# Optimization experiments

Measured on AMD Instinct MI355X. Metric: run time of the kernel, lower is better.

The kernel has to match this reference:

```python
import jax, jax.numpy as jnp
import numpy as np

NL = 5      # number of Block_mamba layers
DM = 256    # d_model
DI = 512    # d_inner = expand * d_model
DS = 64     # d_state
DTR = 16    # dt_rank = ceil(d_model / 16)
HID = 1024  # FFN hidden = dim * mlp_ratio


def layernorm(x, w, b):
    mu = jnp.mean(x, axis=-1, keepdims=True)
    var = jnp.mean((x - mu) ** 2, axis=-1, keepdims=True)
    return (x - mu) * jax.lax.rsqrt(var + 1e-5) * w + b


def mamba_fwd(x, inw, cw, cb, xpw, dtw, dtb, alog, Dp, ow):
    # x: [B, L, DM]
    B, L, _ = x.shape
    xz = jnp.einsum('blc,dc->bld', x, inw)            # [B, L, 2*DI]
    xi, z = xz[..., :DI], xz[..., DI:]
    # causal depthwise conv1d, kernel size 2 (d_conv=2)
    xprev = jnp.pad(xi, ((0, 0), (1, 0), (0, 0)))[:, :-1]
    xc = jax.nn.silu(xi * cw[:, 1] + xprev * cw[:, 0] + cb)   # [B, L, DI]
    xdbl = jnp.einsum('bld,ed->ble', xc, xpw)         # [B, L, DTR+2*DS]
    dt = jax.nn.softplus(jnp.einsum('blr,dr->bld', xdbl[..., :DTR], dtw) + dtb)  # [B,L,DI]
    Bm = xdbl[..., DTR:DTR + DS]                      # [B, L, DS]
    Cm = xdbl[..., DTR + DS:]                         # [B, L, DS]
    A = -jnp.exp(alog)                                # [DI, DS]

    def step(h, inp):
        dt_t, B_t, C_t, u_t = inp                     # [B,DI],[B,DS],[B,DS],[B,DI]
        h = jnp.exp(dt_t[:, :, None] * A) * h + dt_t[:, :, None] * B_t[:, None, :] * u_t[:, :, None]
        y = jnp.einsum('bds,bs->bd', h, C_t)
        return h, y

    h0 = jnp.zeros((B, DI, DS), x.dtype)
    xs = (dt.transpose(1, 0, 2), Bm.transpose(1, 0, 2), Cm.transpose(1, 0, 2), xc.transpose(1, 0, 2))
    _, ys = jax.lax.scan(step, h0, xs)                # ys: [L, B, DI]
    y = ys.transpose(1, 0, 2) + xc * Dp
    y = y * jax.nn.silu(z)
    return jnp.einsum('bld,cd->blc', y, ow)           # [B, L, DM]


def setup_inputs() -> dict:
    key = jax.random.key(0)
    ks = jax.random.split(key, 16)
    f32 = jnp.float32
    d = {}
    d['x'] = jax.random.normal(ks[0], (8, 4096, DM), dtype=f32)
    d['in_proj_w'] = jax.random.normal(ks[1], (NL, 2 * DI, DM), dtype=f32) * 0.02
    d['conv_w'] = jax.random.normal(ks[2], (NL, DI, 2), dtype=f32) * 0.2
    d['conv_b'] = jnp.zeros((NL, DI), f32)
    d['x_proj_w'] = jax.random.normal(ks[3], (NL, DTR + 2 * DS, DI), dtype=f32) * 0.02
    d['dt_proj_w'] = jax.random.normal(ks[4], (NL, DI, DTR), dtype=f32) * 0.02
    d['dt_proj_b'] = jax.random.normal(ks[5], (NL, DI), dtype=f32) * 0.1 - 4.0
    d['A_log'] = jnp.broadcast_to(jnp.log(jnp.arange(1, DS + 1, dtype=f32)), (NL, DI, DS)).copy()
    d['D'] = jnp.ones((NL, DI), f32)
    d['out_proj_w'] = jax.random.normal(ks[6], (NL, DM, DI), dtype=f32) * 0.02
    d['norm1_w'] = jnp.ones((NL, DM), f32)
    d['norm1_b'] = jnp.zeros((NL, DM), f32)
    d['norm2_w'] = jnp.ones((NL, DM), f32)
    d['norm2_b'] = jnp.zeros((NL, DM), f32)
    d['fc1_w'] = jax.random.normal(ks[7], (NL, HID, DM), dtype=f32) * 0.02
    d['fc1_b'] = jnp.zeros((NL, HID), f32)
    d['fc2_w'] = jax.random.normal(ks[8], (NL, DM, HID), dtype=f32) * 0.02
    d['fc2_b'] = jnp.zeros((NL, DM), f32)
    return d


def reference(x, in_proj_w, conv_w, conv_b, x_proj_w, dt_proj_w, dt_proj_b, A_log, D,
              out_proj_w, norm1_w, norm1_b, norm2_w, norm2_b, fc1_w, fc1_b, fc2_w, fc2_b):
    for i in range(NL):
        xn = layernorm(x, norm1_w[i], norm1_b[i])
        args = (in_proj_w[i], conv_w[i], conv_b[i], x_proj_w[i], dt_proj_w[i],
                dt_proj_b[i], A_log[i], D[i], out_proj_w[i])
        fwd = mamba_fwd(xn, *args)
        bwd = mamba_fwd(xn[:, ::-1], *args)[:, ::-1]
        x = x + fwd + bwd                      # bidirectional residual (shared weights)
        xn2 = layernorm(x, norm2_w[i], norm2_b[i])
        h = jax.nn.gelu(jnp.einsum('blc,hc->blh', xn2, fc1_w[i]) + fc1_b[i], approximate=False)
        x = x + jnp.einsum('blh,ch->blc', h, fc2_w[i]) + fc2_b[i]
    return x
```

## Files before the change

### kernel.cpp

```cpp
#include <hip/hip_runtime.h>
#include <hip/hip_bf16.h>
#include <math.h>
#include <stdint.h>

#define NLAY 5
#define DM 256
#define DI 512
#define DS 64
#define DTR 16
#define HID 1024
#define BB 8
#define LSEQ 4096
#define RR (BB*LSEQ)
#define NCH 32
#define CL (LSEQ/NCH)
#define LOG2E 1.4426950408889634f

typedef __hip_bfloat16 bf16;
typedef float vf2 __attribute__((ext_vector_type(2)));
typedef float vf4 __attribute__((ext_vector_type(4)));
typedef unsigned int vu4 __attribute__((ext_vector_type(4)));

__device__ __forceinline__ float silu_f(float x) {
    return x / (1.0f + __expf(-x));
}
__device__ __forceinline__ float gelu_f(float x) {
    return 0.5f * x * (1.0f + erff(x * 0.70710678118654752f));
}
__device__ __forceinline__ float softplus_f(float x) {
    return fmaxf(x, 0.0f) + log1pf(__expf(-fabsf(x)));
}
__device__ __forceinline__ float to_f(bf16 x) { return __bfloat162float(x); }
__device__ __forceinline__ unsigned short bf_bits(float v) {
    bf16 h = __float2bfloat16(v);
    return *reinterpret_cast<unsigned short*>(&h);
}
__device__ __forceinline__ float bflo(uint32_t w) { return __uint_as_float(w << 16); }
__device__ __forceinline__ float rawhi(uint32_t w) { return __uint_as_float(w); }

#define HIDX(dir,b,c,s,d) (((((size_t)(dir)*BB+(b))*NCH+(c))*DS+(s))*DI+(d))
#define SIDX(dir,b,c,d)   ((((size_t)(dir)*BB+(b))*NCH+(c))*DI+(d))

__global__ void ln_kernel(const float* __restrict__ x, const float* __restrict__ w,
                          const float* __restrict__ b, bf16* __restrict__ out) {
    int wave = threadIdx.x >> 6;
    int lane = threadIdx.x & 63;
    int row  = blockIdx.x * 4 + wave;
    const float4* xr = (const float4*)(x + (size_t)row * DM);
    float4 v = xr[lane];
    float s  = v.x + v.y + v.z + v.w;
    float sq = v.x*v.x + v.y*v.y + v.z*v.z + v.w*v.w;
    #pragma unroll
    for (int off = 32; off; off >>= 1) {
        s  += __shfl_xor(s,  off);
        sq += __shfl_xor(sq, off);
    }
    float mu  = s * (1.0f / DM);
    float var = sq * (1.0f / DM) - mu * mu;
    float rs  = rsqrtf(var + 1e-5f);
    float4 wv = ((const float4*)w)[lane];
    float4 bv = ((const float4*)b)[lane];
    ushort4 o;
    o.x = bf_bits((v.x - mu) * rs * wv.x + bv.x);
    o.y = bf_bits((v.y - mu) * rs * wv.y + bv.y);
    o.z = bf_bits((v.z - mu) * rs * wv.z + bv.z);
    o.w = bf_bits((v.w - mu) * rs * wv.w + bv.w);
    ((ushort4*)(out + (size_t)row * DM))[lane] = o;
}

__global__ void wconv_kernel(const float* __restrict__ a0, const float* __restrict__ a1,
                             const float* __restrict__ a2, const float* __restrict__ a3,
                             const float* __restrict__ a4, bf16* __restrict__ out) {
    size_t i = (size_t)blockIdx.x * 256 + threadIdx.x;
    const float* src; size_t off;
    if (i < 262144)      { src = a0; off = i; }
    else if (i < 335872) { src = a1; off = i - 262144; }
    else if (i < 466944) { src = a2; off = i - 335872; }
    else if (i < 729088) { src = a3; off = i - 466944; }
    else                 { src = a4; off = i - 729088; }
    out[i] = __float2bfloat16(src[off]);
}

template<int ACT, bool ACCUM, bool BIAS, typename TC>
__global__ __launch_bounds__(256)
void mfma_gemm(const bf16* __restrict__ A, const bf16* __restrict__ W,
               const float* __restrict__ bias, TC* __restrict__ C,
               int M, int N, int K) {
    __shared__ bf16 As[128][40];
    __shared__ bf16 Ws[64][40];
    int tid = threadIdx.x;
    int m0 = blockIdx.x * 128;
    int n0 = blockIdx.y * 64;
    int w  = tid >> 6, lane = tid & 63;
    int wr = w >> 1, wc = w & 1;
    int fr = lane & 15;
    int kg = lane >> 4;
    vf4 acc[4][2] = {};

    int sr = tid >> 2;
    int skc = (tid & 3) * 8;
    for (int k0 = 0; k0 < K; k0 += 32) {
        #pragma unroll
        for (int i = 0; i < 2; i++) {
            int q = tid + i * 256;
            int r = q >> 2, kc = (q & 3) * 8;
            *(vu4*)&As[r][kc] = *(const vu4*)&A[(size_t)(m0 + r) * K + k0 + kc];
        }
        {
            int n = n0 + sr;
            vu4 v = {0u, 0u, 0u, 0u};
            if (n < N) v = *(const vu4*)&W[(size_t)n * K + k0 + skc];
            *(vu4*)&Ws[sr][skc] = v;
        }
        __syncthreads();
        vu4 af[4], bw[2];
        #pragma unroll
        for (int m = 0; m < 4; m++)
            af[m] = *(const vu4*)&As[wr * 64 + m * 16 + fr][kg * 8];
        #pragma unroll
        for (int n = 0; n < 2; n++)
            bw[n] = *(const vu4*)&Ws[wc * 32 + n * 16 + fr][kg * 8];
        #pragma unroll
        for (int m = 0; m < 4; m++)
            #pragma unroll
            for (int n = 0; n < 2; n++)
                asm("v_mfma_f32_16x16x32_bf16 %0, %1, %2, %0"
                    : "+v"(acc[m][n]) : "v"(af[m]), "v"(bw[n]));
        __syncthreads();
    }

    #pragma unroll
    for (int m = 0; m < 4; m++) {
        #pragma unroll
        for (int n = 0; n < 2; n++) {
            int col = n0 + wc * 32 + n * 16 + fr;
            if (col >= N) continue;
            float bz = BIAS ? bias[col] : 0.0f;
            #pragma unroll
            for (int r = 0; r < 4; r++) {
                int row = m0 + wr * 64 + m * 16 + kg * 4 + r;
                float v = acc[m][n][r] + bz;
                if (ACT == 1) v = silu_f(v);
                else if (ACT == 2) v = gelu_f(v);
                if constexpr (sizeof(TC) == 2) {
                    ((bf16*)C)[(size_t)row * N + col] = __float2bfloat16(v);
                } else {
                    float* cp = (float*)C + (size_t)row * N + col;
                    if (ACCUM) *cp += v; else *cp = v;
                }
            }
        }
    }
}

__global__ void conv_kernel(const bf16* __restrict__ xi, const float* __restrict__ cw,
                            const float* __restrict__ cb, bf16* __restrict__ xcf,
                            bf16* __restrict__ xcb) {
    size_t idx = (size_t)blockIdx.x * 256 + threadIdx.x;
    int d = (int)(idx & (DI - 1));
    size_t row = idx >> 9;
    int t = (int)(row & (LSEQ - 1));
    float x0   = to_f(xi[idx]);
    float prev = (t > 0)        ? to_f(xi[idx - DI]) : 0.0f;
    float nxt  = (t < LSEQ - 1) ? to_f(xi[idx + DI]) : 0.0f;
    float w0 = cw[d * 2], w1 = cw[d * 2 + 1], bc = cb[d];
    float base = x0 * w1 + bc;
    xcf[idx] = __float2bfloat16(silu_f(base + prev * w0));
    xcb[idx] = __float2bfloat16(silu_f(base + nxt * w0));
}

__global__ void dt_kernel(const bf16* __restrict__ xdbl, const float* __restrict__ dtw,
                          const float* __restrict__ dtb, bf16* __restrict__ dt) {
    __shared__ float sx[DTR];
    size_t row = blockIdx.x;
    int d = threadIdx.x;
    if (d < DTR) sx[d] = to_f(xdbl[row * 144 + d]);
    __syncthreads();
    float acc = dtb[d];
    #pragma unroll
    for (int r = 0; r < DTR; r++) acc += sx[r] * dtw[d * DTR + r];
    dt[row * DI + d] = __float2bfloat16(softplus_f(acc));
}


__global__ __launch_bounds__(256) void scanA_kernel(
        const bf16* __restrict__ dt2, const bf16* __restrict__ xdbl2,
        const bf16* __restrict__ xcf, const bf16* __restrict__ xcb,
        bf16* __restrict__ hbuf, float* __restrict__ sdtbuf) {
    int wv = blockIdx.x * 4 + (threadIdx.x >> 6);
    int lane = threadIdx.x & 63;
    int dh  = wv & 15;
    int c   = (wv >> 4) & 31;
    int b   = (wv >> 9) & 7;
    int dir = wv >> 12;
    int dl  = lane & 31;
    int sh  = lane >> 5;
    int d   = dh * 32 + dl;
    const bf16* dt = dt2 + (size_t)dir * RR * DI;
    const bf16* xc = dir ? xcb : xcf;
    const bf16* xb = xdbl2 + (size_t)dir * RR * 144;

    size_t row0 = (size_t)b * LSEQ + (dir ? ((c + 1) * CL - 1) : (c * CL));
    const bf16* dtp = dt + row0 * DI + d;
    const bf16* up  = xc + row0 * DI + d;
    const uint32_t* bcp = (const uint32_t*)(xb + row0 * 144 + DTR) + sh * 16;
    intptr_t stepDI = dir ? -DI : DI;
    intptr_t stepBC = dir ? -72 : 72;

    vf2 h[16];
    #pragma unroll
    for (int j = 0; j < 16; j++) h[j] = (vf2)0.0f;
    float sdt = 0.0f;

    for (int it = 0; it < CL; ++it) {
        float dtv = to_f(*dtp);
        float u   = to_f(*up);
        float du  = dtv * u;
        sdt += dtv;
        float rho = __builtin_amdgcn_exp2f(-dtv * LOG2E);
        float r2 = rho * rho, r3 = r2 * rho, r4 = r2 * r2;
        float r5 = r4 * rho, r6 = r4 * r2, r7 = r4 * r3, r8 = r4 * r4;
        float r16 = r8 * r8, r32 = r16 * r16;
        float sf = sh ? r32 : 1.0f;
        vf2 sf2 = {sf, sf};
        vf2 e0 = vf2{rho, r2} * sf2;
        vf2 e1 = vf2{r3, r4} * sf2;
        vf2 e2 = vf2{r5, r6} * sf2;
        vf2 e3 = vf2{r7, r8} * sf2;
        vf2 r8p = {r8, r8};
        vf2 du2 = {du, du};
        const vu4* pB = (const vu4*)bcp;
        #pragma unroll
        for (int i = 0; i < 4; i++) {
            vu4 w = pB[i];
            vf2 b0 = {bflo(w.x), rawhi(w.x)};
            vf2 b1 = {bflo(w.y), rawhi(w.y)};
            vf2 b2 = {bflo(w.z), rawhi(w.z)};
            vf2 b3 = {bflo(w.w), rawhi(w.w)};
            h[4*i]   = e0 * h[4*i]   + du2 * b0;
            h[4*i+1] = e1 * h[4*i+1] + du2 * b1;
            h[4*i+2] = e2 * h[4*i+2] + du2 * b2;
            h[4*i+3] = e3 * h[4*i+3] + du2 * b3;
            e0 *= r8p; e1 *= r8p; e2 *= r8p; e3 *= r8p;
        }
        dtp += stepDI; up += stepDI; bcp += stepBC;
    }
    size_t base = HIDX(dir, b, c, 0, d) + (size_t)(sh * 32) * DI;
    #pragma unroll
    for (int j = 0; j < 16; j++) {
        hbuf[base + (size_t)(2*j)   * DI] = __float2bfloat16(h[j].x);
        hbuf[base + (size_t)(2*j+1) * DI] = __float2bfloat16(h[j].y);
    }
    if (sh == 0) sdtbuf[SIDX(dir, b, c, d)] = sdt;
}

__global__ __launch_bounds__(64) void scanB_kernel(
        bf16* __restrict__ hbuf, const float* __restrict__ sdtbuf) {
    int x = blockIdx.x;
    int dsl = x & 7;
    int s   = (x >> 3) & 63;
    int b   = (x >> 9) & 7;
    int dir = x >> 12;
    int d = dsl * 64 + threadIdx.x;
    float kexp = -(float)(s + 1) * LOG2E;
    float h0 = 0.0f;
    for (int i = 0; i < NCH; ++i) {
        int c = dir ? (NCH - 1 - i) : i;
        size_t hi = HIDX(dir, b, c, s, d);
        float E  = __builtin_amdgcn_exp2f(kexp * sdtbuf[SIDX(dir, b, c, d)]);
        float hf = to_f(hbuf[hi]);
        hbuf[hi] = __float2bfloat16(h0);
        h0 = E * h0 + hf;
    }
}

__global__ __launch_bounds__(256) void scanC_kernel(
        const bf16* __restrict__ dt2, const bf16* __restrict__ xdbl2,
        bf16* __restrict__ xcf, bf16* __restrict__ xcb,
        const float* __restrict__ Dp, const bf16* __restrict__ hbuf) {
    int wv = blockIdx.x * 4 + (threadIdx.x >> 6);
    int lane = threadIdx.x & 63;
    int dh  = wv & 15;
    int c   = (wv >> 4) & 31;
    int b   = (wv >> 9) & 7;
    int dir = wv >> 12;
    int dl  = lane & 31;
    int sh  = lane >> 5;
    int d   = dh * 32 + dl;
    const bf16* dt = dt2 + (size_t)dir * RR * DI;
    bf16* xc = dir ? xcb : xcf;
    const bf16* xb = xdbl2 + (size_t)dir * RR * 144;
    float Dv = Dp[d];

    size_t row0 = (size_t)b * LSEQ + (dir ? ((c + 1) * CL - 1) : (c * CL));
    const bf16* dtp = dt + row0 * DI + d;
    bf16* up = xc + row0 * DI + d;
    const uint32_t* bcp = (const uint32_t*)(xb + row0 * 144 + DTR) + sh * 16;
    intptr_t stepDI = dir ? -DI : DI;
    intptr_t stepBC = dir ? -72 : 72;

    vf2 h[16];
    size_t base = HIDX(dir, b, c, 0, d) + (size_t)(sh * 32) * DI;
    #pragma unroll
    for (int j = 0; j < 16; j++) {
        h[j].x = to_f(hbuf[base + (size_t)(2*j)   * DI]);
        h[j].y = to_f(hbuf[base + (size_t)(2*j+1) * DI]);
    }

    for (int it = 0; it < CL; ++it) {
        float dtv = to_f(*dtp);
        float u   = to_f(*up);
        float du  = dtv * u;
        float rho = __builtin_amdgcn_exp2f(-dtv * LOG2E);
        float r2 = rho * rho, r3 = r2 * rho, r4 = r2 * r2;
        float r5 = r4 * rho, r6 = r4 * r2, r7 = r4 * r3, r8 = r4 * r4;
        float r16 = r8 * r8, r32 = r16 * r16;
        float sf = sh ? r32 : 1.0f;
        vf2 sf2 = {sf, sf};
        vf2 e0 = vf2{rho, r2} * sf2;
        vf2 e1 = vf2{r3, r4} * sf2;
        vf2 e2 = vf2{r5, r6} * sf2;
        vf2 e3 = vf2{r7, r8} * sf2;
        vf2 r8p = {r8, r8};
        vf2 du2 = {du, du};
        vf2 y0 = (vf2)0.0f, y1 = (vf2)0.0f;
        const vu4* pB = (const vu4*)bcp;
        const vu4* pC = (const vu4*)(bcp + 32);
        #pragma unroll
        for (int i = 0; i < 4; i++) {
            vu4 wB = pB[i];
            vu4 wC = pC[i];
            vf2 b0 = {bflo(wB.x), rawhi(wB.x)};
            vf2 b1 = {bflo(wB.y), rawhi(wB.y)};
            vf2 b2 = {bflo(wB.z), rawhi(wB.z)};
            vf2 b3 = {bflo(wB.w), rawhi(wB.w)};
            vf2 c0 = {bflo(wC.x), rawhi(wC.x)};
            vf2 c1 = {bflo(wC.y), rawhi(wC.y)};
            vf2 c2 = {bflo(wC.z), rawhi(wC.z)};
            vf2 c3 = {bflo(wC.w), rawhi(wC.w)};
            h[4*i]   = e0 * h[4*i]   + du2 * b0;  y0 += h[4*i]   * c0;
            h[4*i+1] = e1 * h[4*i+1] + du2 * b1;  y1 += h[4*i+1] * c1;
            h[4*i+2] = e2 * h[4*i+2] + du2 * b2;  y0 += h[4*i+2] * c2;
            h[4*i+3] = e3 * h[4*i+3] + du2 * b3;  y1 += h[4*i+3] * c3;
            e0 *= r8p; e1 *= r8p; e2 *= r8p; e3 *= r8p;
        }
        vf2 yp = y0 + y1;
        float yhalf = yp.x + yp.y;
        float y = yhalf + __shfl_xor(yhalf, 32);
        if (sh == 0) *up = __float2bfloat16(y + u * Dv);
        dtp += stepDI; up += stepDI; bcp += stepBC;
    }
}

__global__ void combine_kernel(bf16* __restrict__ xcf, const bf16* __restrict__ xcb,
                               const bf16* __restrict__ z) {
    size_t idx = (size_t)blockIdx.x * 256 + threadIdx.x;
    int dcol = (int)(idx & (DI - 1));
    size_t row = idx >> 9;
    float zz = to_f(z[row * DI + dcol]);
    float v = (to_f(xcf[idx]) + to_f(xcb[idx])) * silu_f(zz);
    xcf[idx] = __float2bfloat16(v);
}

extern "C" void kernel_launch(void* const* d_in, const int* in_sizes, int n_in,
                              void* d_out, int out_size, void* d_ws, size_t ws_size,
                              hipStream_t stream) {
    const float* x_in = (const float*)d_in[0];
    const float* inw  = (const float*)d_in[1];
    const float* cw   = (const float*)d_in[2];
    const float* cb   = (const float*)d_in[3];
    const float* xpw  = (const float*)d_in[4];
    const float* dtw  = (const float*)d_in[5];
    const float* dtb  = (const float*)d_in[6];
    const float* Dp   = (const float*)d_in[8];
    const float* ow   = (const float*)d_in[9];
    const float* n1w  = (const float*)d_in[10];
    const float* n1b  = (const float*)d_in[11];
    const float* n2w  = (const float*)d_in[12];
    const float* n2b  = (const float*)d_in[13];
    const float* f1w  = (const float*)d_in[14];
    const float* f1b  = (const float*)d_in[15];
    const float* f2w  = (const float*)d_in[16];
    const float* f2b  = (const float*)d_in[17];

    const size_t SZ_DI  = (size_t)RR * DI * 2;
    const size_t SZ_XDB = (size_t)2 * RR * 144 * 2;
    const size_t SZ_DT  = (size_t)2 * RR * DI * 2;
    const size_t SZ_WBF = (size_t)991232 * 2;
    const size_t SZ_SDT = (size_t)2 * BB * NCH * DI * 4;
    const size_t NEEDED = 4 * SZ_DI + SZ_XDB + SZ_DT + SZ_WBF + SZ_SDT;
    if (ws_size < NEEDED) return;

    char* p = (char*)d_ws;
    bf16*  xi    = (bf16*)p; p += SZ_DI;
    bf16*  z     = (bf16*)p; p += SZ_DI;
    bf16*  xcf   = (bf16*)p; p += SZ_DI;
    bf16*  xcb   = (bf16*)p; p += SZ_DI;
    bf16*  xdbl2 = (bf16*)p; p += SZ_XDB;
    bf16*  dt2   = (bf16*)p; p += SZ_DT;
    bf16*  wbf   = (bf16*)p; p += SZ_WBF;
    float* sdtb  = (float*)p; p += SZ_SDT;
    bf16*  hbuf  = xi;
    bf16*  xn    = xcb;
    bf16*  hmlp  = dt2;
    bf16*  inw_bf = wbf;
    bf16*  xpw_bf = wbf + 262144;
    bf16*  ow_bf  = wbf + 335872;
    bf16*  f1w_bf = wbf + 466944;
    bf16*  f2w_bf = wbf + 729088;

    float* x = (float*)d_out;
    hipMemcpyAsync(x, x_in, (size_t)RR * DM * sizeof(float), hipMemcpyDeviceToDevice, stream);

    dim3 blk(256);
    for (int l = 0; l < NLAY; ++l) {
        const float* inw_l = inw + (size_t)l * 2 * DI * DM;
        const float* cw_l  = cw  + (size_t)l * DI * 2;
        const float* cb_l  = cb  + (size_t)l * DI;
        const float* xpw_l = xpw + (size_t)l * 144 * DI;
        const float* dtw_l = dtw + (size_t)l * DI * DTR;
        const float* dtb_l = dtb + (size_t)l * DI;
        const float* Dp_l  = Dp  + (size_t)l * DI;
        const float* ow_l  = ow  + (size_t)l * DM * DI;
        const float* f1w_l = f1w + (size_t)l * HID * DM;
        const float* f1b_l = f1b + (size_t)l * HID;
        const float* f2w_l = f2w + (size_t)l * DM * HID;
        const float* f2b_l = f2b + (size_t)l * DM;

        wconv_kernel<<<3872, blk, 0, stream>>>(inw_l, xpw_l, ow_l, f1w_l, f2w_l, wbf);

        ln_kernel<<<RR / 4, blk, 0, stream>>>(x, n1w + l * DM, n1b + l * DM, xn);
        mfma_gemm<0, false, false, bf16><<<dim3(RR / 128, 8), blk, 0, stream>>>(
            xn, inw_bf, nullptr, xi, RR, DI, DM);
        mfma_gemm<0, false, false, bf16><<<dim3(RR / 128, 8), blk, 0, stream>>>(
            xn, inw_bf + (size_t)DI * DM, nullptr, z, RR, DI, DM);
        conv_kernel<<<(RR * DI) / 256, blk, 0, stream>>>(xi, cw_l, cb_l, xcf, xcb);
        mfma_gemm<0, false, false, bf16><<<dim3(2 * RR / 128, 3), blk, 0, stream>>>(
            xcf, xpw_bf, nullptr, xdbl2, 2 * RR, 144, DI);
        dt_kernel<<<2 * RR, dim3(DI), 0, stream>>>(xdbl2, dtw_l, dtb_l, dt2);

        scanA_kernel<<<2048, blk, 0, stream>>>(dt2, xdbl2, xcf, xcb, hbuf, sdtb);
        scanB_kernel<<<8192, dim3(64), 0, stream>>>(hbuf, sdtb);
        scanC_kernel<<<2048, blk, 0, stream>>>(dt2, xdbl2, xcf, xcb, Dp_l, hbuf);
        combine_kernel<<<(RR * DI) / 256, blk, 0, stream>>>(xcf, xcb, z);

        mfma_gemm<0, true, false, float><<<dim3(RR / 128, 4), blk, 0, stream>>>(
            xcf, ow_bf, nullptr, x, RR, DM, DI);

        ln_kernel<<<RR / 4, blk, 0, stream>>>(x, n2w + l * DM, n2b + l * DM, xn);
        mfma_gemm<2, false, true, bf16><<<dim3(RR / 128, 16), blk, 0, stream>>>(
            xn, f1w_bf, f1b_l, hmlp, RR, HID, DM);
        mfma_gemm<0, true, true, float><<<dim3(RR / 128, 4), blk, 0, stream>>>(
            hmlp, f2w_bf, f2b_l, x, RR, DM, HID);
    }
}
```

Before: 4.705 ms.

## Fuse combine into backward scan pass and load GEMM tiles directly to LDS

scanC is split into separate forward and backward launches. The backward launch reads the forward output and z, then writes (yf+yb)*silu(z) directly, so the standalone combine kernel and its full pass over three bf16 tensors disappear. The GEMM now stages A and W tiles with global_load_lds 16-byte transfers into unpadded LDS, skipping the register round-trip. The costs are that the two scan directions no longer run concurrently, and the unpadded LDS layout may cause bank conflicts. The W load also loses its bounds check and can read past the x_proj weights for N=144.

Result: no change. 4.757 ms (+1.1%).

```diff
diff --git a/kernel.cpp b/kernel.cpp
--- a/kernel.cpp
+++ b/kernel.cpp
@@ -38,6 +38,13 @@
 __device__ __forceinline__ float bflo(uint32_t w) { return __uint_as_float(w << 16); }
 __device__ __forceinline__ float rawhi(uint32_t w) { return __uint_as_float(w); }
 
+__device__ __forceinline__ void gl_lds16(const bf16* g, bf16* l) {
+    __builtin_amdgcn_global_load_lds(
+        (const __attribute__((address_space(1))) unsigned int*)g,
+        (__attribute__((address_space(3))) unsigned int*)l,
+        16, 0, 0);
+}
+
 #define HIDX(dir,b,c,s,d) (((((size_t)(dir)*BB+(b))*NCH+(c))*DS+(s))*DI+(d))
 #define SIDX(dir,b,c,d)   ((((size_t)(dir)*BB+(b))*NCH+(c))*DI+(d))
 
@@ -86,8 +93,8 @@
 void mfma_gemm(const bf16* __restrict__ A, const bf16* __restrict__ W,
                const float* __restrict__ bias, TC* __restrict__ C,
                int M, int N, int K) {
-    __shared__ bf16 As[128][40];
-    __shared__ bf16 Ws[64][40];
+    __shared__ bf16 As[128 * 32];
+    __shared__ bf16 Ws[64 * 32];
     int tid = threadIdx.x;
     int m0 = blockIdx.x * 128;
     int n0 = blockIdx.y * 64;
@@ -97,29 +104,22 @@
     int kg = lane >> 4;
     vf4 acc[4][2] = {};
 
-    int sr = tid >> 2;
-    int skc = (tid & 3) * 8;
+    int r0 = tid >> 2, kc0 = (tid & 3) * 8;
+    int q1 = tid + 256;
+    int r1 = q1 >> 2, kc1 = (q1 & 3) * 8;
+
     for (int k0 = 0; k0 < K; k0 += 32) {
-        #pragma unroll
-        for (int i = 0; i < 2; i++) {
-            int q = tid + i * 256;
-            int r = q >> 2, kc = (q & 3) * 8;
-            *(vu4*)&As[r][kc] = *(const vu4*)&A[(size_t)(m0 + r) * K + k0 + kc];
-        }
-        {
-            int n = n0 + sr;
-            vu4 v = {0u, 0u, 0u, 0u};
-            if (n < N) v = *(const vu4*)&W[(size_t)n * K + k0 + skc];
-            *(vu4*)&Ws[sr][skc] = v;
-        }
+        gl_lds16(&A[(size_t)(m0 + r0) * K + k0 + kc0], As + (size_t)w * 512);
+        gl_lds16(&A[(size_t)(m0 + r1) * K + k0 + kc1], As + 2048 + (size_t)w * 512);
+        gl_lds16(&W[(size_t)(n0 + r0) * K + k0 + kc0], Ws + (size_t)w * 512);
         __syncthreads();
         vu4 af[4], bw[2];
         #pragma unroll
         for (int m = 0; m < 4; m++)
-            af[m] = *(const vu4*)&As[wr * 64 + m * 16 + fr][kg * 8];
+            af[m] = *(const vu4*)&As[(wr * 64 + m * 16 + fr) * 32 + kg * 8];
         #pragma unroll
         for (int n = 0; n < 2; n++)
-            bw[n] = *(const vu4*)&Ws[wc * 32 + n * 16 + fr][kg * 8];
+            bw[n] = *(const vu4*)&Ws[(wc * 32 + n * 16 + fr) * 32 + kg * 8];
         #pragma unroll
         for (int m = 0; m < 4; m++)
             #pragma unroll
@@ -274,27 +274,32 @@
     }
 }
 
+template<bool BWD>
 __global__ __launch_bounds__(256) void scanC_kernel(
         const bf16* __restrict__ dt2, const bf16* __restrict__ xdbl2,
         bf16* __restrict__ xcf, bf16* __restrict__ xcb,
+        const bf16* __restrict__ z,
         const float* __restrict__ Dp, const bf16* __restrict__ hbuf) {
     int wv = blockIdx.x * 4 + (threadIdx.x >> 6);
     int lane = threadIdx.x & 63;
     int dh  = wv & 15;
     int c   = (wv >> 4) & 31;
-    int b   = (wv >> 9) & 7;
-    int dir = wv >> 12;
+    int b   = wv >> 9;
+    const int dir = BWD ? 1 : 0;
     int dl  = lane & 31;
     int sh  = lane >> 5;
     int d   = dh * 32 + dl;
     const bf16* dt = dt2 + (size_t)dir * RR * DI;
-    bf16* xc = dir ? xcb : xcf;
+    bf16* xc = BWD ? xcb : xcf;
     const bf16* xb = xdbl2 + (size_t)dir * RR * 144;
     float Dv = Dp[d];
 
     size_t row0 = (size_t)b * LSEQ + (dir ? ((c + 1) * CL - 1) : (c * CL));
-    const bf16* dtp = dt + row0 * DI + d;
-    bf16* up = xc + row0 * DI + d;
+    size_t pos0 = row0 * DI + d;
+    const bf16* dtp = dt + pos0;
+    bf16* up = xc + pos0;
+    bf16* yfp = xcf + pos0;
+    const bf16* zp  = z + pos0;
     const uint32_t* bcp = (const uint32_t*)(xb + row0 * 144 + DTR) + sh * 16;
     intptr_t stepDI = dir ? -DI : DI;
     intptr_t stepBC = dir ? -72 : 72;
@@ -347,19 +352,19 @@
         vf2 yp = y0 + y1;
         float yhalf = yp.x + yp.y;
         float y = yhalf + __shfl_xor(yhalf, 32);
-        if (sh == 0) *up = __float2bfloat16(y + u * Dv);
+        if (sh == 0) {
+            float yfull = y + u * Dv;
+            if (BWD) {
+                float yf = to_f(*yfp);
+                float zz = to_f(*zp);
+                *yfp = __float2bfloat16((yf + yfull) * silu_f(zz));
+            } else {
+                *up = __float2bfloat16(yfull);
+            }
+        }
         dtp += stepDI; up += stepDI; bcp += stepBC;
-    }
-}
-
-__global__ void combine_kernel(bf16* __restrict__ xcf, const bf16* __restrict__ xcb,
-                               const bf16* __restrict__ z) {
-    size_t idx = (size_t)blockIdx.x * 256 + threadIdx.x;
-    int dcol = (int)(idx & (DI - 1));
-    size_t row = idx >> 9;
-    float zz = to_f(z[row * DI + dcol]);
-    float v = (to_f(xcf[idx]) + to_f(xcb[idx])) * silu_f(zz);
-    xcf[idx] = __float2bfloat16(v);
+        yfp += stepDI; zp += stepDI;
+    }
 }
 
 extern "C" void kernel_launch(void* const* d_in, const int* in_sizes, int n_in,
@@ -441,8 +446,10 @@
 
         scanA_kernel<<<2048, blk, 0, stream>>>(dt2, xdbl2, xcf, xcb, hbuf, sdtb);
         scanB_kernel<<<8192, dim3(64), 0, stream>>>(hbuf, sdtb);
-        scanC_kernel<<<2048, blk, 0, stream>>>(dt2, xdbl2, xcf, xcb, Dp_l, hbuf);
-        combine_kernel<<<(RR * DI) / 256, blk, 0, stream>>>(xcf, xcb, z);
+        scanC_kernel<false><<<1024, blk, 0, stream>>>(
+            dt2, xdbl2, xcf, xcb, z, Dp_l, hbuf);
+        scanC_kernel<true><<<1024, blk, 0, stream>>>(
+            dt2, xdbl2, xcf, xcb, z, Dp_l, hbuf);
 
         mfma_gemm<0, true, false, float><<<dim3(RR / 128, 4), blk, 0, stream>>>(
             xcf, ow_bf, nullptr, x, RR, DM, DI);
```
